# Optimization experiments

Measured on AMD Instinct MI355X. Metric: run time of the kernel, lower is better.

Reference implementation:

```python
import jax, jax.numpy as jnp
import numpy as np

N_NODES = 50000
N_EDGES = 800000
D_IN = 128
D_OUT = 128


def setup_inputs() -> dict:
    key = jax.random.key(0)
    k1, k2, k3, k4 = jax.random.split(key, 4)
    feature = jax.random.normal(k1, (N_NODES, D_IN), dtype=jnp.float32)
    edge_src = jax.random.randint(k2, (N_EDGES,), 0, N_NODES, dtype=jnp.int32)
    edge_dst = jax.random.randint(k3, (N_EDGES,), 0, N_NODES, dtype=jnp.int32)
    W = jax.random.normal(k4, (D_IN, D_OUT), dtype=jnp.float32) * (1.0 / np.sqrt(D_IN))
    b = jnp.zeros((D_OUT,), dtype=jnp.float32)
    return {"feature": feature, "edge_src": edge_src, "edge_dst": edge_dst, "W": W, "b": b}


def reference(feature, edge_src, edge_dst, W, b):
    # copy_src + sum reduce: for each edge, copy src node feature, sum into dst node
    msgs = feature[edge_src]  # [E, D_IN] gather
    h = jax.ops.segment_sum(msgs, edge_dst, num_segments=N_NODES)  # [N, D_IN]
    # linear + activation (relu)
    return jax.nn.relu(h @ W + b)
```

## Files before the change

### kernel.cpp

```cpp
#include <hip/hip_runtime.h>
#include <hip/hip_fp16.h>


constexpr int N    = 50000;
constexpr int E    = 800000;
constexpr int D    = 128;
constexpr int CAP  = 64;
constexpr int NT   = 3125;
constexpr int ZSTR = 136;
constexpr int NR   = 782;
constexpr int HB   = 500;
constexpr int EPB  = E / HB;

using f16x8 = __attribute__((ext_vector_type(8))) _Float16;
using f32x4 = __attribute__((ext_vector_type(4))) float;

__global__ void setup(const float* __restrict__ W, _Float16* __restrict__ Wf,
                      _Float16* __restrict__ Z) {
    if (blockIdx.x == 8) {
        if (threadIdx.x < D) Z[(size_t)N * D + threadIdx.x] = (_Float16)0.f;
        return;
    }
    int t = blockIdx.x * 256 + threadIdx.x;
    int ct = t >> 8, ks = (t >> 6) & 3, lane = t & 63;
    int q = lane >> 4, li = lane & 15;
    _Float16 v[8];
    #pragma unroll
    for (int j = 0; j < 8; ++j)
        v[j] = (_Float16)W[(ks * 32 + q * 8 + j) * D + ct * 16 + li];
    *(f16x8*)(Wf + (size_t)t * 8) = *(const f16x8*)v;
}

__global__ __launch_bounds__(256) void midk(
        const float* __restrict__ feature,
        const int*   __restrict__ edst,
        const _Float16* __restrict__ Wf,
        int* __restrict__ hist,
        _Float16* __restrict__ Z) {
    __shared__ int h[NR];
    __shared__ _Float16 zs[4][16 * ZSTR];
    const int tid = threadIdx.x;

    if (blockIdx.x < HB) {
        const int b = blockIdx.x;
        for (int i = tid; i < NR; i += 256) h[i] = 0;
        __syncthreads();
        const int e0 = b * EPB;
        for (int i = tid; i < EPB; i += 256)
            atomicAdd(&h[edst[e0 + i] >> 6], 1);
        __syncthreads();
        for (int i = tid; i < NR; i += 256) hist[b * NR + i] = h[i];
        return;
    }

    const int wave = tid >> 6, lane = tid & 63;
    const int wt = (blockIdx.x - HB) * 4 + wave;
    if (wt >= NT) return;
    const int q = lane >> 4, li = lane & 15;

    const float* fp = feature + (size_t)(wt * 16 + li) * D + q * 8;
    f16x8 afr[4];
    #pragma unroll
    for (int ks = 0; ks < 4; ++ks) {
        const float4 u0 = *(const float4*)(fp + ks * 32);
        const float4 u1 = *(const float4*)(fp + ks * 32 + 4);
        afr[ks][0] = (_Float16)u0.x; afr[ks][1] = (_Float16)u0.y;
        afr[ks][2] = (_Float16)u0.z; afr[ks][3] = (_Float16)u0.w;
        afr[ks][4] = (_Float16)u1.x; afr[ks][5] = (_Float16)u1.y;
        afr[ks][6] = (_Float16)u1.z; afr[ks][7] = (_Float16)u1.w;
    }

    f32x4 acc[8];
    #pragma unroll
    for (int ct = 0; ct < 8; ++ct) acc[ct] = (f32x4){0.f, 0.f, 0.f, 0.f};
    #pragma unroll
    for (int ks = 0; ks < 4; ++ks)
        #pragma unroll
        for (int ct = 0; ct < 8; ++ct) {
            const f16x8 b = *(const f16x8*)(Wf + (size_t)((ct * 4 + ks) * 64 + lane) * 8);
            acc[ct] = __builtin_amdgcn_mfma_f32_16x16x32_f16(afr[ks], b, acc[ct], 0, 0, 0);
        }

    _Float16* zt = zs[wave];
    #pragma unroll
    for (int ct = 0; ct < 8; ++ct)
        #pragma unroll
        for (int r = 0; r < 4; ++r)
            zt[(q * 4 + r) * ZSTR + ct * 16 + li] = (_Float16)acc[ct][r];
    #pragma unroll
    for (int it = 0; it < 4; ++it) {
        const f16x8 v = *(const f16x8*)(zt + (it * 4 + q) * ZSTR + li * 8);
        *(f16x8*)(Z + (size_t)(wt * 16 + it * 4 + q) * D + li * 8) = v;
    }
}

__global__ void scank(int* __restrict__ hist, int* __restrict__ total) {
    const int r    = blockIdx.x;
    const int lane = threadIdx.x;
    int h[8], sum = 0;
    #pragma unroll
    for (int j = 0; j < 8; ++j) {
        const int idx = lane * 8 + j;
        h[j] = (idx < HB) ? hist[idx * NR + r] : 0;
        sum += h[j];
    }
    int incl = sum;
    #pragma unroll
    for (int off = 1; off < 64; off <<= 1) {
        int u = __shfl_up(incl, off);
        if (lane >= off) incl += u;
    }
    int run = incl - sum;
    #pragma unroll
    for (int j = 0; j < 8; ++j) {
        const int idx = lane * 8 + j;
        if (idx < HB) hist[idx * NR + r] = run;
        run += h[j];
    }
    if (lane == 63) total[r] = run;
}

__global__ __launch_bounds__(256) void partk(
        const int* __restrict__ esrc,
        const int* __restrict__ edst,
        const int* __restrict__ blockBase,
        const int* __restrict__ total,
        int* __restrict__ rangeStartG,
        unsigned int* __restrict__ part) {
    __shared__ int rs[NR];
    __shared__ int mb[NR];
    __shared__ int rk[NR];
    const int tid = threadIdx.x;
    const int b   = blockIdx.x;

    if (tid < 64) {
        int carry = 0;
        #pragma unroll
        for (int c = 0; c < 13; ++c) {
            const int idx = c * 64 + tid;
            const int v = (idx < NR) ? total[idx] : 0;
            int incl = v;
            #pragma unroll
            for (int off = 1; off < 64; off <<= 1) {
                int u = __shfl_up(incl, off);
                if (tid >= off) incl += u;
            }
            if (idx < NR) rs[idx] = incl - v + carry;
            carry += __shfl(incl, 63);
        }
    }
    for (int i = tid; i < NR; i += 256) { mb[i] = blockBase[b * NR + i]; rk[i] = 0; }
    __syncthreads();
    if (b == 0)
        for (int i = tid; i < NR; i += 256) rangeStartG[i] = rs[i];

    const int e0 = b * EPB;
    for (int i = tid; i < EPB; i += 256) {
        const int s = esrc[e0 + i];
        const int d = edst[e0 + i];
        const int r = d >> 6;
        const int k = atomicAdd(&rk[r], 1);
        part[rs[r] + mb[r] + k] = ((unsigned)(d & 63) << 16) | (unsigned)s;
    }
}

__global__ __launch_bounds__(256) void csrgather(
        const unsigned int* __restrict__ part,
        const int* __restrict__ rangeStart,
        const int* __restrict__ total,
        const _Float16* __restrict__ Z,
        const float* __restrict__ bias,
        float* __restrict__ out) {
    __shared__ unsigned short bkt[32 * CAP];
    __shared__ int deg[32];
    const int r   = blockIdx.x >> 1;
    const int sub = blockIdx.x & 1;
    const int tid = threadIdx.x;

    if (tid < 32) deg[tid] = 0;
    __syncthreads();
    const int rsv = rangeStart[r], tot = total[r];
    for (int i = tid; i < tot; i += 256) {
        const unsigned p = part[rsv + i];
        const int local = p >> 16;
        if ((local >> 5) == sub) {
            const int l5 = local & 31;
            const int k = atomicAdd(&deg[l5], 1);
            if (k < CAP) bkt[l5 * CAP + k] = (unsigned short)(p & 0xFFFF);
        }
    }
    __syncthreads();

    const int wave = tid >> 6, lane = tid & 63;
    const int g = lane >> 4, li = lane & 15;
    const float4 b0 = *(const float4*)(bias + li * 8);
    const float4 b1 = *(const float4*)(bias + li * 8 + 4);

    for (int pair = 0; pair < 4; ++pair) {
        const int lA = wave * 8 + pair * 2;
        const int lB = lA + 1;
        const int degA = min(deg[lA], CAP);
        const int degB = min(deg[lB], CAP);

        float accA[8] = {0,0,0,0,0,0,0,0};
        float accB[8] = {0,0,0,0,0,0,0,0};

        const int mx = max(degA, degB);
        for (int base = 0; base < mx; base += 16) {
            f16x8 hA[4], hB[4];
            #pragma unroll
            for (int t = 0; t < 4; ++t) {
                const int rr = base + t * 4 + g;
                int sA = bkt[lA * CAP + rr];
                int sB = bkt[lB * CAP + rr];
                sA = (rr < degA) ? sA : N;
                sB = (rr < degB) ? sB : N;
                hA[t] = *(const f16x8*)(Z + (size_t)sA * D + li * 8);
                hB[t] = *(const f16x8*)(Z + (size_t)sB * D + li * 8);
            }
            #pragma unroll
            for (int t = 0; t < 4; ++t)
                #pragma unroll
                for (int j = 0; j < 8; ++j) {
                    accA[j] += (float)hA[t][j];
                    accB[j] += (float)hB[t][j];
                }
        }

        #pragma unroll
        for (int j = 0; j < 8; ++j) {
            accA[j] += __shfl_xor(accA[j], 16);
            accA[j] += __shfl_xor(accA[j], 32);
            accB[j] += __shfl_xor(accB[j], 16);
            accB[j] += __shfl_xor(accB[j], 32);
        }

        const int nodeA = (r << 6) + (sub << 5) + lA;
        const int nodeB = nodeA + 1;
        if (g == 0 && nodeA < N) {
            float4 o0, o1;
            o0.x = fmaxf(accA[0] + b0.x, 0.f); o0.y = fmaxf(accA[1] + b0.y, 0.f);
            o0.z = fmaxf(accA[2] + b0.z, 0.f); o0.w = fmaxf(accA[3] + b0.w, 0.f);
            o1.x = fmaxf(accA[4] + b1.x, 0.f); o1.y = fmaxf(accA[5] + b1.y, 0.f);
            o1.z = fmaxf(accA[6] + b1.z, 0.f); o1.w = fmaxf(accA[7] + b1.w, 0.f);
            float* op = out + (size_t)nodeA * D + li * 8;
            *(float4*)op       = o0;
            *(float4*)(op + 4) = o1;
        } else if (g == 1 && nodeB < N) {
            float4 o0, o1;
            o0.x = fmaxf(accB[0] + b0.x, 0.f); o0.y = fmaxf(accB[1] + b0.y, 0.f);
            o0.z = fmaxf(accB[2] + b0.z, 0.f); o0.w = fmaxf(accB[3] + b0.w, 0.f);
            o1.x = fmaxf(accB[4] + b1.x, 0.f); o1.y = fmaxf(accB[5] + b1.y, 0.f);
            o1.z = fmaxf(accB[6] + b1.z, 0.f); o1.w = fmaxf(accB[7] + b1.w, 0.f);
            float* op = out + (size_t)nodeB * D + li * 8;
            *(float4*)op       = o0;
            *(float4*)(op + 4) = o1;
        }
    }
}

extern "C" void kernel_launch(void* const* d_in, const int* in_sizes, int n_in,
                              void* d_out, int out_size, void* d_ws, size_t ws_size,
                              hipStream_t stream) {
    const float* feature = (const float*)d_in[0];
    const int*   esrc    = (const int*)d_in[1];
    const int*   edst    = (const int*)d_in[2];
    const float* W       = (const float*)d_in[3];
    const float* bias    = (const float*)d_in[4];
    float*       out     = (float*)d_out;

    _Float16*     Z      = (_Float16*)d_ws;
    _Float16*     Wf     = Z + (size_t)(N + 1) * D;
    int*          hist   = (int*)(Wf + 16384);
    int*          total  = hist + HB * NR;
    int*          rangeS = total + NR;
    unsigned int* part   = (unsigned int*)(rangeS + NR);

    setup<<<9, 256, 0, stream>>>(W, Wf, Z);
    midk <<<HB + (NT + 3) / 4, 256, 0, stream>>>(feature, edst, Wf, hist, Z);
    scank<<<NR, 64, 0, stream>>>(hist, total);
    partk<<<HB, 256, 0, stream>>>(esrc, edst, hist, total, rangeS, part);
    csrgather<<<NR * 2, 256, 0, stream>>>(part, rangeS, total, Z, bias, out);
}
```

Before: 143.3 us.

## Sort nodes by degree and gather four nodes per wave in csrgather

After bucketing edges, each block ranks its 32 nodes by in-degree and processes them in sorted order, four nodes per wave iteration instead of two. Grouping nodes of similar degree cuts the idle lanes caused by padding every node to the group's max degree, and having more gathers in flight per iteration raises memory-level parallelism. It also adds a launch-bounds occupancy hint. The costs are a small ranking pass with an extra barrier and higher register pressure from four accumulator sets.

```diff
diff --git a/kernel.cpp b/kernel.cpp
--- a/kernel.cpp
+++ b/kernel.cpp
@@ -164,7 +164,7 @@
     }
 }
 
-__global__ __launch_bounds__(256) void csrgather(
+__global__ __launch_bounds__(256, 4) void csrgather(
         const unsigned int* __restrict__ part,
         const int* __restrict__ rangeStart,
         const int* __restrict__ total,
@@ -173,6 +173,7 @@
         float* __restrict__ out) {
     __shared__ unsigned short bkt[32 * CAP];
     __shared__ int deg[32];
+    __shared__ unsigned char perm[32];
     const int r   = blockIdx.x >> 1;
     const int sub = blockIdx.x & 1;
     const int tid = threadIdx.x;
@@ -191,68 +192,89 @@
     }
     __syncthreads();
 
+    if (tid < 32) {
+        const int d = deg[tid];
+        int rk = 0;
+        for (int j = 0; j < 32; ++j) {
+            const int dj = deg[j];
+            rk += (dj > d) || (dj == d && j < tid);
+        }
+        perm[rk] = (unsigned char)tid;
+    }
+    __syncthreads();
+
     const int wave = tid >> 6, lane = tid & 63;
     const int g = lane >> 4, li = lane & 15;
-    const float4 b0 = *(const float4*)(bias + li * 8);
-    const float4 b1 = *(const float4*)(bias + li * 8 + 4);
-
-    for (int pair = 0; pair < 4; ++pair) {
-        const int lA = wave * 8 + pair * 2;
-        const int lB = lA + 1;
-        const int degA = min(deg[lA], CAP);
-        const int degB = min(deg[lB], CAP);
-
-        float accA[8] = {0,0,0,0,0,0,0,0};
-        float accB[8] = {0,0,0,0,0,0,0,0};
-
-        const int mx = max(degA, degB);
+
+    #pragma unroll 1
+    for (int grp = 0; grp < 2; ++grp) {
+        const int l0 = perm[wave * 8 + grp * 4 + 0];
+        const int l1 = perm[wave * 8 + grp * 4 + 1];
+        const int l2 = perm[wave * 8 + grp * 4 + 2];
+        const int l3 = perm[wave * 8 + grp * 4 + 3];
+        const int d0 = min(deg[l0], CAP), d1 = min(deg[l1], CAP);
+        const int d2 = min(deg[l2], CAP), d3 = min(deg[l3], CAP);
+
+        float a0[8] = {0,0,0,0,0,0,0,0};
+        float a1[8] = {0,0,0,0,0,0,0,0};
+        float a2[8] = {0,0,0,0,0,0,0,0};
+        float a3[8] = {0,0,0,0,0,0,0,0};
+
+        const int mx = max(max(d0, d1), max(d2, d3));
+        #pragma unroll 1
         for (int base = 0; base < mx; base += 16) {
-            f16x8 hA[4], hB[4];
+            f16x8 h0[4], h1[4], h2[4], h3[4];
             #pragma unroll
             for (int t = 0; t < 4; ++t) {
                 const int rr = base + t * 4 + g;
-                int sA = bkt[lA * CAP + rr];
-                int sB = bkt[lB * CAP + rr];
-                sA = (rr < degA) ? sA : N;
-                sB = (rr < degB) ? sB : N;
-                hA[t] = *(const f16x8*)(Z + (size_t)sA * D + li * 8);
-                hB[t] = *(const f16x8*)(Z + (size_t)sB * D + li * 8);
+                int s0 = bkt[l0 * CAP + rr];
+                int s1 = bkt[l1 * CAP + rr];
+                int s2 = bkt[l2 * CAP + rr];
+                int s3 = bkt[l3 * CAP + rr];
+                s0 = (rr < d0) ? s0 : N;
+                s1 = (rr < d1) ? s1 : N;
+                s2 = (rr < d2) ? s2 : N;
+                s3 = (rr < d3) ? s3 : N;
+                h0[t] = *(const f16x8*)(Z + (size_t)s0 * D + li * 8);
+                h1[t] = *(const f16x8*)(Z + (size_t)s1 * D + li * 8);
+                h2[t] = *(const f16x8*)(Z + (size_t)s2 * D + li * 8);
+                h3[t] = *(const f16x8*)(Z + (size_t)s3 * D + li * 8);
             }
             #pragma unroll
             for (int t = 0; t < 4; ++t)
                 #pragma unroll
                 for (int j = 0; j < 8; ++j) {
-                    accA[j] += (float)hA[t][j];
-                    accB[j] += (float)hB[t][j];
+                    a0[j] += (float)h0[t][j];
+                    a1[j] += (float)h1[t][j];
+                    a2[j] += (float)h2[t][j];
+                    a3[j] += (float)h3[t][j];
                 }
         }
 
         #pragma unroll
         for (int j = 0; j < 8; ++j) {
-            accA[j] += __shfl_xor(accA[j], 16);
-            accA[j] += __shfl_xor(accA[j], 32);
-            accB[j] += __shfl_xor(accB[j], 16);
-            accB[j] += __shfl_xor(accB[j], 32);
-        }
-
-        const int nodeA = (r << 6) + (sub << 5) + lA;
-        const int nodeB = nodeA + 1;
-        if (g == 0 && nodeA < N) {
+            a0[j] += __shfl_xor(a0[j], 16); a0[j] += __shfl_xor(a0[j], 32);
+            a1[j] += __shfl_xor(a1[j], 16); a1[j] += __shfl_xor(a1[j], 32);
+            a2[j] += __shfl_xor(a2[j], 16); a2[j] += __shfl_xor(a2[j], 32);
+            a3[j] += __shfl_xor(a3[j], 16); a3[j] += __shfl_xor(a3[j], 32);
+        }
+
+        const int ln = (g == 0) ? l0 : (g == 1) ? l1 : (g == 2) ? l2 : l3;
+        float av[8];
+        #pragma unroll
+        for (int j = 0; j < 8; ++j)
+            av[j] = (g == 0) ? a0[j] : (g == 1) ? a1[j] : (g == 2) ? a2[j] : a3[j];
+
+        const int node = (r << 6) + (sub << 5) + ln;
+        if (node < N) {
+            const float4 b0 = *(const float4*)(bias + li * 8);
+            const float4 b1 = *(const float4*)(bias + li * 8 + 4);
             float4 o0, o1;
-            o0.x = fmaxf(accA[0] + b0.x, 0.f); o0.y = fmaxf(accA[1] + b0.y, 0.f);
-            o0.z = fmaxf(accA[2] + b0.z, 0.f); o0.w = fmaxf(accA[3] + b0.w, 0.f);
-            o1.x = fmaxf(accA[4] + b1.x, 0.f); o1.y = fmaxf(accA[5] + b1.y, 0.f);
-            o1.z = fmaxf(accA[6] + b1.z, 0.f); o1.w = fmaxf(accA[7] + b1.w, 0.f);
-            float* op = out + (size_t)nodeA * D + li * 8;
-            *(float4*)op       = o0;
-            *(float4*)(op + 4) = o1;
-        } else if (g == 1 && nodeB < N) {
-            float4 o0, o1;
-            o0.x = fmaxf(accB[0] + b0.x, 0.f); o0.y = fmaxf(accB[1] + b0.y, 0.f);
-            o0.z = fmaxf(accB[2] + b0.z, 0.f); o0.w = fmaxf(accB[3] + b0.w, 0.f);
-            o1.x = fmaxf(accB[4] + b1.x, 0.f); o1.y = fmaxf(accB[5] + b1.y, 0.f);
-            o1.z = fmaxf(accB[6] + b1.z, 0.f); o1.w = fmaxf(accB[7] + b1.w, 0.f);
-            float* op = out + (size_t)nodeB * D + li * 8;
+            o0.x = fmaxf(av[0] + b0.x, 0.f); o0.y = fmaxf(av[1] + b0.y, 0.f);
+            o0.z = fmaxf(av[2] + b0.z, 0.f); o0.w = fmaxf(av[3] + b0.w, 0.f);
+            o1.x = fmaxf(av[4] + b1.x, 0.f); o1.y = fmaxf(av[5] + b1.y, 0.f);
+            o1.z = fmaxf(av[6] + b1.z, 0.f); o1.w = fmaxf(av[7] + b1.w, 0.f);
+            float* op = out + (size_t)node * D + li * 8;
             *(float4*)op       = o0;
             *(float4*)(op + 4) = o1;
         }
```

New measurement: 145.6 us. Within noise of the previous version (+1.6%).
